# Kernel tuning notes

Measured on AMD Instinct MI355X. Metric: run time of the kernel, lower is better.

Reference implementation:

```python
import jax, jax.numpy as jnp
import numpy as np

INPUT_DIM, HIDDEN_DIM, OUTPUT_DIM = 13, 256, 80


def setup_inputs() -> dict:
    key = jax.random.key(0)
    ks = jax.random.split(key, 5)
    x = jax.random.normal(ks[0], (64, 2048, INPUT_DIM), dtype=jnp.float32)
    # Xavier-uniform init like init_weights(); biases zero.
    def xavier(k, fan_in, fan_out):
        lim = np.sqrt(6.0 / (fan_in + fan_out)).astype(np.float32)
        return jax.random.uniform(k, (fan_in, fan_out), jnp.float32, -lim, lim)
    W1 = xavier(ks[1], INPUT_DIM, HIDDEN_DIM)
    W2 = xavier(ks[2], HIDDEN_DIM, HIDDEN_DIM)
    W3 = xavier(ks[3], HIDDEN_DIM, HIDDEN_DIM)
    W4 = xavier(ks[4], HIDDEN_DIM, OUTPUT_DIM)
    b1 = jnp.zeros((HIDDEN_DIM,), jnp.float32)
    b2 = jnp.zeros((HIDDEN_DIM,), jnp.float32)
    b3 = jnp.zeros((HIDDEN_DIM,), jnp.float32)
    b4 = jnp.zeros((OUTPUT_DIM,), jnp.float32)
    return {"x": x, "W1": W1, "b1": b1, "W2": W2, "b2": b2,
            "W3": W3, "b3": b3, "W4": W4, "b4": b4}


def reference(x, W1, b1, W2, b2, W3, b3, W4, b4):
    # Original loops over timesteps, but each timestep is an identical
    # Linear+ReLU stack -> collapse batch*seq into one batched matmul chain.
    h = jax.nn.relu(jnp.einsum('bsi,ih->bsh', x, W1) + b1)   # encoder L1
    h = jax.nn.relu(jnp.einsum('bsh,hk->bsk', h, W2) + b2)   # encoder L2
    h = jax.nn.relu(jnp.einsum('bsh,hk->bsk', h, W3) + b3)   # decoder L1
    out = jnp.einsum('bsh,ho->bso', h, W4) + b4              # decoder L2 (no ReLU)
    return out
```

## Files before the change

kernel.cpp:

```cpp
#include <hip/hip_runtime.h>


typedef _Float16 half_t;
typedef _Float16 half8 __attribute__((ext_vector_type(8)));
typedef float f32x16 __attribute__((ext_vector_type(16)));
typedef unsigned int uint4v __attribute__((ext_vector_type(4)));
typedef int int2v __attribute__((ext_vector_type(2)));

#define M_TOTAL (64*2048)

__global__ void prep_w(const float* __restrict__ W1, const float* __restrict__ W2,
                       const float* __restrict__ W3, const float* __restrict__ W4,
                       half_t* __restrict__ wp) {
    int tid = blockIdx.x * 256 + threadIdx.x;
    if (tid >= 312 * 512) return;
    int blk = tid >> 9, r = tid & 511;
    int lane = r >> 3, j = r & 7;
    const float* W; int K, N, nt, ks;
    if (blk < 8)        { W = W1; K = 13;  N = 256; nt = blk;              ks = 0; }
    else if (blk < 136) { W = W2; K = 256; N = 256; nt = (blk-8) >> 4;     ks = (blk-8) & 15; }
    else if (blk < 264) { W = W3; K = 256; N = 256; nt = (blk-136) >> 4;   ks = (blk-136) & 15; }
    else                { W = W4; K = 256; N = 80;  nt = (blk-264) >> 4;   ks = (blk-264) & 15; }
    int k = ks * 16 + (lane >> 5) * 8 + j;
    int n = nt * 32 + (lane & 31);
    float v = (k < K && n < N) ? W[k * N + n] : 0.f;
    wp[tid] = (half_t)v;
}


__device__ __forceinline__ unsigned int pkrtz(float a, float b) {
    auto p = __builtin_amdgcn_cvt_pkrtz(a, b);
    return __builtin_bit_cast(unsigned int, p);
}

typedef const __attribute__((address_space(1))) unsigned int guint_t;
typedef __attribute__((address_space(3))) unsigned int luint_t;

__device__ __forceinline__ void stage_strip(const half_t* __restrict__ g,
                                            half_t* l, int bytes, int tid) {
    const char* gc = (const char*)g;
    char* lc = (char*)l;
    const int go = tid * 16;
    const int lo = (tid >> 6) << 10;
#pragma unroll
    for (int r = 0; r < bytes; r += 8192) {
        __builtin_amdgcn_global_load_lds((guint_t*)(gc + r + go),
                                         (luint_t*)(lc + r + lo), 16, 0, 0);
    }
}

__device__ __forceinline__ int strip_off(int s) {
    if (s == 0)  return 0;
    if (s <= 8)  return (8   + (s - 1)  * 16) * 512;
    if (s <= 16) return (136 + (s - 9)  * 16) * 512;
    return (264 + (s - 17) * 16) * 512;
}

#define PIPE_BAR(Nstr) do {                                   \
    asm volatile("s_waitcnt vmcnt(" Nstr ")" ::: "memory");   \
    __builtin_amdgcn_sched_barrier(0);                        \
    __builtin_amdgcn_s_barrier();                             \
    __builtin_amdgcn_sched_barrier(0);                        \
} while (0)

template <int NKS, bool RELU>
__device__ __forceinline__ void dense_tile(const half_t* astrip,
                                           const unsigned int (&Bin)[16][4],
                                           unsigned int (*Bout)[4],
                                           const float* biasnt, int lane, bool hi)
{
    f32x16 acc = {};
    __builtin_amdgcn_s_setprio(1);
#pragma unroll
    for (int ks = 0; ks < NKS; ++ks) {
        half8 a = *(const half8*)(astrip + ((ks * 64 + lane) << 3));
        uint4v bw = { Bin[ks][0], Bin[ks][1], Bin[ks][2], Bin[ks][3] };
        acc = __builtin_amdgcn_mfma_f32_32x32x16_f16(a, __builtin_bit_cast(half8, bw),
                                                     acc, 0, 0, 0);
    }
    __builtin_amdgcn_s_setprio(0);
#pragma unroll
    for (int s = 0; s < 2; ++s) {
        float v[8];
#pragma unroll
        for (int q = 0; q < 8; ++q) {
            int f = (q & 3) + 8 * (q >> 2) + (hi ? 4 : 0);
            float t = acc[8 * s + q] + biasnt[16 * s + f];
            v[q] = RELU ? fmaxf(t, 0.f) : t;
        }
        unsigned int P0 = pkrtz(v[0], v[1]);
        unsigned int P1 = pkrtz(v[2], v[3]);
        unsigned int P2 = pkrtz(v[4], v[5]);
        unsigned int P3 = pkrtz(v[6], v[7]);
        int2v r02 = __builtin_amdgcn_permlane32_swap((int)P0, (int)P2, false, false);
        int2v r13 = __builtin_amdgcn_permlane32_swap((int)P1, (int)P3, false, false);
        Bout[s][0] = (unsigned int)r02.x;
        Bout[s][1] = (unsigned int)r13.x;
        Bout[s][2] = (unsigned int)r02.y;
        Bout[s][3] = (unsigned int)r13.y;
    }
}

__device__ __forceinline__ void out_tile(const half_t* astrip,
                                         const unsigned int (&Bin)[16][4],
                                         const float* biasnt, float* __restrict__ out,
                                         int m0, int nt, int lane, bool hi)
{
    f32x16 acc = {};
    __builtin_amdgcn_s_setprio(1);
#pragma unroll
    for (int ks = 0; ks < 16; ++ks) {
        half8 a = *(const half8*)(astrip + ((ks * 64 + lane) << 3));
        uint4v bw = { Bin[ks][0], Bin[ks][1], Bin[ks][2], Bin[ks][3] };
        acc = __builtin_amdgcn_mfma_f32_32x32x16_f16(a, __builtin_bit_cast(half8, bw),
                                                     acc, 0, 0, 0);
    }
    __builtin_amdgcn_s_setprio(0);
    float* orow = out + (long)(m0 + (lane & 31)) * 80 + nt * 32;
#pragma unroll
    for (int reg = 0; reg < 16; ++reg) {
        if (nt == 2 && (reg >> 2) >= 2) continue;
        int rr = (reg & 3) + 8 * (reg >> 2) + (hi ? 4 : 0);
        orow[rr] = acc[reg] + biasnt[rr];
    }
}

__global__ __launch_bounds__(512, 2) void mlp_mfma(
    const float* __restrict__ x, const half_t* __restrict__ wp,
    const float* __restrict__ b1, const float* __restrict__ b2,
    const float* __restrict__ b3, const float* __restrict__ b4,
    float* __restrict__ out)
{
    __shared__ half_t wbuf[3][8192];
    __shared__ float  bias_lds[864];

    const int tid  = threadIdx.x;
    const int lane = tid & 63;
    const bool hi  = lane >= 32;
    const int m0   = (blockIdx.x * 8 + (tid >> 6)) * 32;

    if (tid < 256) {
        bias_lds[tid] = b1[tid];
        bias_lds[256 + tid] = b2[tid];
        bias_lds[512 + tid] = b3[tid];
    } else if (tid < 352) {
        int t = tid - 256;
        bias_lds[768 + t] = (t < 80) ? b4[t] : 0.f;
    }

    stage_strip(wp + strip_off(0), wbuf[0], 8192, tid);
    stage_strip(wp + strip_off(1), wbuf[1], 16384, tid);

    unsigned int BA[16][4], BB[16][4];

    {
        const float* xp = x + (long)(m0 + (lane & 31)) * 13;
        float xv[8];
        if (!hi) {
#pragma unroll
            for (int j = 0; j < 8; ++j) xv[j] = xp[j];
        } else {
#pragma unroll
            for (int j = 0; j < 5; ++j) xv[j] = xp[8 + j];
            xv[5] = xv[6] = xv[7] = 0.f;
        }
        BA[0][0] = pkrtz(xv[0], xv[1]);
        BA[0][1] = pkrtz(xv[2], xv[3]);
        BA[0][2] = pkrtz(xv[4], xv[5]);
        BA[0][3] = pkrtz(xv[6], xv[7]);
    }

    __syncthreads();

    stage_strip(wp + strip_off(2), wbuf[2], 16384, tid);
#pragma unroll
    for (int nt = 0; nt < 8; ++nt)
        dense_tile<1, true>(&wbuf[0][nt * 512], BA, &BB[2 * nt],
                            bias_lds + nt * 32, lane, hi);

#pragma unroll
    for (int i = 0; i < 8; ++i) {
        const int k = 1 + i;
        PIPE_BAR("2");
        stage_strip(wp + strip_off(k + 2), wbuf[(k + 2) % 3], 16384, tid);
        dense_tile<16, true>(&wbuf[k % 3][0], BB, &BA[2 * i],
                             bias_lds + 256 + i * 32, lane, hi);
    }

#pragma unroll
    for (int i = 0; i < 8; ++i) {
        const int k = 9 + i;
        PIPE_BAR("2");
        stage_strip(wp + strip_off(k + 2), wbuf[(k + 2) % 3], 16384, tid);
        dense_tile<16, true>(&wbuf[k % 3][0], BA, &BB[2 * i],
                             bias_lds + 512 + i * 32, lane, hi);
    }

#pragma unroll
    for (int i = 0; i < 3; ++i) {
        const int k = 17 + i;
        if (i < 2) PIPE_BAR("2");
        else       PIPE_BAR("0");
        if (i == 0) stage_strip(wp + strip_off(19), wbuf[19 % 3], 16384, tid);
        out_tile(&wbuf[k % 3][0], BB, bias_lds + 768 + i * 32, out, m0, i, lane, hi);
    }
}


extern "C" void kernel_launch(void* const* d_in, const int* in_sizes, int n_in,
                              void* d_out, int out_size, void* d_ws, size_t ws_size,
                              hipStream_t stream) {
    const float* x  = (const float*)d_in[0];
    const float* W1 = (const float*)d_in[1];
    const float* b1 = (const float*)d_in[2];
    const float* W2 = (const float*)d_in[3];
    const float* b2 = (const float*)d_in[4];
    const float* W3 = (const float*)d_in[5];
    const float* b3 = (const float*)d_in[6];
    const float* W4 = (const float*)d_in[7];
    const float* b4 = (const float*)d_in[8];
    float* out = (float*)d_out;

    half_t* wp = (half_t*)d_ws;

    hipLaunchKernelGGL(prep_w, dim3(624), dim3(256), 0, stream, W1, W2, W3, W4, wp);
    hipLaunchKernelGGL(mlp_mfma, dim3(M_TOTAL / 256), dim3(512), 0, stream,
                       x, wp, b1, b2, b3, b4, out);
}
```

Measured before the change: 54.21 us.

## Fold biases into MFMA via augmented K, use 1024-thread blocks with half-layer staging

Biases are folded into the weight matrices as an extra K row, paired with a constant-one input column, and applied through an additional MFMA per tile, so the separate bias LDS loads and adds go away. Blocks grow to 1024 threads (16 waves, 512 rows), which halves how many times each block stages the weights. Staging now moves half a layer (4 N-tiles) per step into a 2-buffer, roughly 144 KB LDS, replacing the triple-buffered per-strip pipeline, so there are fewer barriers. In exchange there is less overlap between loads and compute, since every step waits on vmcnt(0), occupancy drops to one block per CU, and each tile does about 6% more MFMA work.

```diff
diff --git a/kernel.cpp b/kernel.cpp
--- a/kernel.cpp
+++ b/kernel.cpp
@@ -8,22 +8,33 @@
 typedef int int2v __attribute__((ext_vector_type(2)));
 
 #define M_TOTAL (64*2048)
-
-__global__ void prep_w(const float* __restrict__ W1, const float* __restrict__ W2,
-                       const float* __restrict__ W3, const float* __restrict__ W4,
+#define NBLK 331
+
+#define L2_OFF (8*512)
+#define L3_OFF (144*512)
+#define L4_OFF (280*512)
+#define HSTRIP (17*4*512)
+
+__global__ void prep_w(const float* __restrict__ W1, const float* __restrict__ b1,
+                       const float* __restrict__ W2, const float* __restrict__ b2,
+                       const float* __restrict__ W3, const float* __restrict__ b3,
+                       const float* __restrict__ W4, const float* __restrict__ b4,
                        half_t* __restrict__ wp) {
     int tid = blockIdx.x * 256 + threadIdx.x;
-    if (tid >= 312 * 512) return;
-    int blk = tid >> 9, r = tid & 511;
-    int lane = r >> 3, j = r & 7;
-    const float* W; int K, N, nt, ks;
-    if (blk < 8)        { W = W1; K = 13;  N = 256; nt = blk;              ks = 0; }
-    else if (blk < 136) { W = W2; K = 256; N = 256; nt = (blk-8) >> 4;     ks = (blk-8) & 15; }
-    else if (blk < 264) { W = W3; K = 256; N = 256; nt = (blk-136) >> 4;   ks = (blk-136) & 15; }
-    else                { W = W4; K = 256; N = 80;  nt = (blk-264) >> 4;   ks = (blk-264) & 15; }
+    if (tid >= NBLK * 512) return;
+    int blk = tid >> 9, r = tid & 511, lane = r >> 3, j = r & 7;
+    const float* W; const float* bias; int K, N, nt, ks;
+    if (blk < 8)        { W = W1; bias = b1; K = 13;  N = 256; nt = blk; ks = 0; }
+    else if (blk < 144) { int b = blk - 8;   W = W2; bias = b2; K = 256; N = 256; nt = b / 17; ks = b % 17; }
+    else if (blk < 280) { int b = blk - 144; W = W3; bias = b3; K = 256; N = 256; nt = b / 17; ks = b % 17; }
+    else                { int b = blk - 280; W = W4; bias = b4; K = 256; N = 80;  nt = b / 17; ks = b % 17; }
     int k = ks * 16 + (lane >> 5) * 8 + j;
     int n = nt * 32 + (lane & 31);
-    float v = (k < K && n < N) ? W[k * N + n] : 0.f;
+    float v = 0.f;
+    if (n < N) {
+        if (k < K)       v = W[k * N + n];
+        else if (k == K) v = bias[n];
+    }
     wp[tid] = (half_t)v;
 }
 
@@ -36,56 +47,47 @@
 typedef const __attribute__((address_space(1))) unsigned int guint_t;
 typedef __attribute__((address_space(3))) unsigned int luint_t;
 
-__device__ __forceinline__ void stage_strip(const half_t* __restrict__ g,
-                                            half_t* l, int bytes, int tid) {
+__device__ __forceinline__ void stage(const half_t* __restrict__ g,
+                                      half_t* l, int bytes, int tid) {
     const char* gc = (const char*)g;
     char* lc = (char*)l;
     const int go = tid * 16;
     const int lo = (tid >> 6) << 10;
-#pragma unroll
-    for (int r = 0; r < bytes; r += 8192) {
+    int r = 0;
+#pragma unroll
+    for (; r + 16384 <= bytes; r += 16384)
         __builtin_amdgcn_global_load_lds((guint_t*)(gc + r + go),
                                          (luint_t*)(lc + r + lo), 16, 0, 0);
-    }
-}
-
-__device__ __forceinline__ int strip_off(int s) {
-    if (s == 0)  return 0;
-    if (s <= 8)  return (8   + (s - 1)  * 16) * 512;
-    if (s <= 16) return (136 + (s - 9)  * 16) * 512;
-    return (264 + (s - 17) * 16) * 512;
-}
-
-#define PIPE_BAR(Nstr) do {                                   \
-    asm volatile("s_waitcnt vmcnt(" Nstr ")" ::: "memory");   \
+    if ((bytes & 16383) && go < (bytes & 16383))
+        __builtin_amdgcn_global_load_lds((guint_t*)(gc + r + go),
+                                         (luint_t*)(lc + r + lo), 16, 0, 0);
+}
+
+#define PIPE_BAR0 do {                                        \
+    asm volatile("s_waitcnt vmcnt(0)" ::: "memory");          \
     __builtin_amdgcn_sched_barrier(0);                        \
     __builtin_amdgcn_s_barrier();                             \
     __builtin_amdgcn_sched_barrier(0);                        \
 } while (0)
 
-template <int NKS, bool RELU>
-__device__ __forceinline__ void dense_tile(const half_t* astrip,
-                                           const unsigned int (&Bin)[16][4],
-                                           unsigned int (*Bout)[4],
-                                           const float* biasnt, int lane, bool hi)
+#define MFMA16(a, b, c) __builtin_amdgcn_mfma_f32_32x32x16_f16((a), (b), (c), 0, 0, 0)
+
+__device__ __forceinline__ half8 bw_cast(const unsigned int* w) {
+    uint4v t = { w[0], w[1], w[2], w[3] };
+    return __builtin_bit_cast(half8, t);
+}
+
+template <bool RELU>
+__device__ __forceinline__ void repack2(const f32x16& acc, bool hi,
+                                        unsigned int* B0, unsigned int* B1)
 {
-    f32x16 acc = {};
-    __builtin_amdgcn_s_setprio(1);
-#pragma unroll
-    for (int ks = 0; ks < NKS; ++ks) {
-        half8 a = *(const half8*)(astrip + ((ks * 64 + lane) << 3));
-        uint4v bw = { Bin[ks][0], Bin[ks][1], Bin[ks][2], Bin[ks][3] };
-        acc = __builtin_amdgcn_mfma_f32_32x32x16_f16(a, __builtin_bit_cast(half8, bw),
-                                                     acc, 0, 0, 0);
-    }
-    __builtin_amdgcn_s_setprio(0);
 #pragma unroll
     for (int s = 0; s < 2; ++s) {
+        unsigned int* Bw = s ? B1 : B0;
         float v[8];
 #pragma unroll
         for (int q = 0; q < 8; ++q) {
-            int f = (q & 3) + 8 * (q >> 2) + (hi ? 4 : 0);
-            float t = acc[8 * s + q] + biasnt[16 * s + f];
+            float t = acc[8 * s + q];
             v[q] = RELU ? fmaxf(t, 0.f) : t;
         }
         unsigned int P0 = pkrtz(v[0], v[1]);
@@ -94,65 +96,57 @@
         unsigned int P3 = pkrtz(v[6], v[7]);
         int2v r02 = __builtin_amdgcn_permlane32_swap((int)P0, (int)P2, false, false);
         int2v r13 = __builtin_amdgcn_permlane32_swap((int)P1, (int)P3, false, false);
-        Bout[s][0] = (unsigned int)r02.x;
-        Bout[s][1] = (unsigned int)r13.x;
-        Bout[s][2] = (unsigned int)r02.y;
-        Bout[s][3] = (unsigned int)r13.y;
-    }
-}
-
-__device__ __forceinline__ void out_tile(const half_t* astrip,
-                                         const unsigned int (&Bin)[16][4],
-                                         const float* biasnt, float* __restrict__ out,
-                                         int m0, int nt, int lane, bool hi)
+        Bw[0] = (unsigned int)r02.x;
+        Bw[1] = (unsigned int)r13.x;
+        Bw[2] = (unsigned int)r02.y;
+        Bw[3] = (unsigned int)r13.y;
+    }
+}
+
+template <bool RELU>
+__device__ __forceinline__ void dense4(const half_t* rg,
+                                       const unsigned int (&Bin)[16][4],
+                                       unsigned int (&Bout)[16][4],
+                                       int ntbase, int lane, bool hi,
+                                       unsigned int cw)
 {
-    f32x16 acc = {};
-    __builtin_amdgcn_s_setprio(1);
-#pragma unroll
-    for (int ks = 0; ks < 16; ++ks) {
-        half8 a = *(const half8*)(astrip + ((ks * 64 + lane) << 3));
-        uint4v bw = { Bin[ks][0], Bin[ks][1], Bin[ks][2], Bin[ks][3] };
-        acc = __builtin_amdgcn_mfma_f32_32x32x16_f16(a, __builtin_bit_cast(half8, bw),
-                                                     acc, 0, 0, 0);
-    }
-    __builtin_amdgcn_s_setprio(0);
-    float* orow = out + (long)(m0 + (lane & 31)) * 80 + nt * 32;
-#pragma unroll
-    for (int reg = 0; reg < 16; ++reg) {
-        if (nt == 2 && (reg >> 2) >= 2) continue;
-        int rr = (reg & 3) + 8 * (reg >> 2) + (hi ? 4 : 0);
-        orow[rr] = acc[reg] + biasnt[rr];
-    }
-}
-
-__global__ __launch_bounds__(512, 2) void mlp_mfma(
+#pragma unroll
+    for (int t = 0; t < 4; ++t) {
+        const half_t* astrip = rg + t * 17 * 512;
+        f32x16 acc = {};
+        __builtin_amdgcn_s_setprio(1);
+#pragma unroll
+        for (int ks = 0; ks < 16; ++ks) {
+            half8 a = *(const half8*)(astrip + ((ks * 64 + lane) << 3));
+            acc = MFMA16(a, bw_cast(Bin[ks]), acc);
+        }
+        {
+            half8 a = *(const half8*)(astrip + ((16 * 64 + lane) << 3));
+            uint4v cb = { cw, 0u, 0u, 0u };
+            acc = MFMA16(a, __builtin_bit_cast(half8, cb), acc);
+        }
+        __builtin_amdgcn_s_setprio(0);
+        repack2<RELU>(acc, hi, Bout[2 * (ntbase + t)], Bout[2 * (ntbase + t) + 1]);
+    }
+}
+
+__global__ __launch_bounds__(1024, 1) void mlp_mfma(
     const float* __restrict__ x, const half_t* __restrict__ wp,
-    const float* __restrict__ b1, const float* __restrict__ b2,
-    const float* __restrict__ b3, const float* __restrict__ b4,
     float* __restrict__ out)
 {
-    __shared__ half_t wbuf[3][8192];
-    __shared__ float  bias_lds[864];
+    __shared__ half_t lds[73728];
 
     const int tid  = threadIdx.x;
     const int lane = tid & 63;
+    const int wave = tid >> 6;
     const bool hi  = lane >= 32;
-    const int m0   = (blockIdx.x * 8 + (tid >> 6)) * 32;
-
-    if (tid < 256) {
-        bias_lds[tid] = b1[tid];
-        bias_lds[256 + tid] = b2[tid];
-        bias_lds[512 + tid] = b3[tid];
-    } else if (tid < 352) {
-        int t = tid - 256;
-        bias_lds[768 + t] = (t < 80) ? b4[t] : 0.f;
-    }
-
-    stage_strip(wp + strip_off(0), wbuf[0], 8192, tid);
-    stage_strip(wp + strip_off(1), wbuf[1], 16384, tid);
-
-    unsigned int BA[16][4], BB[16][4];
-
+    const int m0   = blockIdx.x * 512 + wave * 32;
+    const unsigned int cw = hi ? 0u : 0x3C00u;
+
+    stage(wp,          lds,         8192,  tid);
+    stage(wp + L2_OFF, lds + 4096,  69632, tid);
+
+    unsigned int Bx[4];
     {
         const float* xp = x + (long)(m0 + (lane & 31)) * 13;
         float xv[8];
@@ -162,47 +156,68 @@
         } else {
 #pragma unroll
             for (int j = 0; j < 5; ++j) xv[j] = xp[8 + j];
-            xv[5] = xv[6] = xv[7] = 0.f;
-        }
-        BA[0][0] = pkrtz(xv[0], xv[1]);
-        BA[0][1] = pkrtz(xv[2], xv[3]);
-        BA[0][2] = pkrtz(xv[4], xv[5]);
-        BA[0][3] = pkrtz(xv[6], xv[7]);
-    }
-
-    __syncthreads();
-
-    stage_strip(wp + strip_off(2), wbuf[2], 16384, tid);
-#pragma unroll
-    for (int nt = 0; nt < 8; ++nt)
-        dense_tile<1, true>(&wbuf[0][nt * 512], BA, &BB[2 * nt],
-                            bias_lds + nt * 32, lane, hi);
-
-#pragma unroll
-    for (int i = 0; i < 8; ++i) {
-        const int k = 1 + i;
-        PIPE_BAR("2");
-        stage_strip(wp + strip_off(k + 2), wbuf[(k + 2) % 3], 16384, tid);
-        dense_tile<16, true>(&wbuf[k % 3][0], BB, &BA[2 * i],
-                             bias_lds + 256 + i * 32, lane, hi);
-    }
-
-#pragma unroll
-    for (int i = 0; i < 8; ++i) {
-        const int k = 9 + i;
-        PIPE_BAR("2");
-        stage_strip(wp + strip_off(k + 2), wbuf[(k + 2) % 3], 16384, tid);
-        dense_tile<16, true>(&wbuf[k % 3][0], BA, &BB[2 * i],
-                             bias_lds + 512 + i * 32, lane, hi);
-    }
-
-#pragma unroll
-    for (int i = 0; i < 3; ++i) {
-        const int k = 17 + i;
-        if (i < 2) PIPE_BAR("2");
-        else       PIPE_BAR("0");
-        if (i == 0) stage_strip(wp + strip_off(19), wbuf[19 % 3], 16384, tid);
-        out_tile(&wbuf[k % 3][0], BB, bias_lds + 768 + i * 32, out, m0, i, lane, hi);
+            xv[5] = 1.0f;
+            xv[6] = xv[7] = 0.f;
+        }
+        Bx[0] = pkrtz(xv[0], xv[1]);
+        Bx[1] = pkrtz(xv[2], xv[3]);
+        Bx[2] = pkrtz(xv[4], xv[5]);
+        Bx[3] = pkrtz(xv[6], xv[7]);
+    }
+
+    PIPE_BAR0;
+
+    unsigned int BA[16][4], BB[16][4];
+
+    stage(wp + L2_OFF + HSTRIP, lds + 38912, 69632, tid);
+    {
+        half8 bx = bw_cast(Bx);
+#pragma unroll
+        for (int nt = 0; nt < 8; ++nt) {
+            half8 a = *(const half8*)(lds + nt * 512 + (lane << 3));
+            f32x16 acc = {};
+            acc = MFMA16(a, bx, acc);
+            repack2<true>(acc, hi, BB[2 * nt], BB[2 * nt + 1]);
+        }
+    }
+    dense4<true>(lds + 4096, BB, BA, 0, lane, hi, cw);
+    PIPE_BAR0;
+
+    stage(wp + L3_OFF, lds + 4096, 69632, tid);
+    dense4<true>(lds + 38912, BB, BA, 4, lane, hi, cw);
+    PIPE_BAR0;
+
+    stage(wp + L3_OFF + HSTRIP, lds + 38912, 69632, tid);
+    dense4<true>(lds + 4096, BA, BB, 0, lane, hi, cw);
+    PIPE_BAR0;
+
+    stage(wp + L4_OFF, lds + 4096, 52224, tid);
+    dense4<true>(lds + 38912, BA, BB, 4, lane, hi, cw);
+    PIPE_BAR0;
+
+#pragma unroll
+    for (int t = 0; t < 3; ++t) {
+        const half_t* astrip = lds + 4096 + t * 17 * 512;
+        f32x16 acc = {};
+        __builtin_amdgcn_s_setprio(1);
+#pragma unroll
+        for (int ks = 0; ks < 16; ++ks) {
+            half8 a = *(const half8*)(astrip + ((ks * 64 + lane) << 3));
+            acc = MFMA16(a, bw_cast(BB[ks]), acc);
+        }
+        {
+            half8 a = *(const half8*)(astrip + ((16 * 64 + lane) << 3));
+            uint4v cb = { cw, 0u, 0u, 0u };
+            acc = MFMA16(a, __builtin_bit_cast(half8, cb), acc);
+        }
+        __builtin_amdgcn_s_setprio(0);
+        float* orow = out + (long)(m0 + (lane & 31)) * 80 + t * 32;
+#pragma unroll
+        for (int reg = 0; reg < 16; ++reg) {
+            if (t == 2 && (reg >> 2) >= 2) continue;
+            int rr = (reg & 3) + 8 * (reg >> 2) + (hi ? 4 : 0);
+            orow[rr] = acc[reg];
+        }
     }
 }
 
@@ -223,7 +238,8 @@
 
     half_t* wp = (half_t*)d_ws;
 
-    hipLaunchKernelGGL(prep_w, dim3(624), dim3(256), 0, stream, W1, W2, W3, W4, wp);
-    hipLaunchKernelGGL(mlp_mfma, dim3(M_TOTAL / 256), dim3(512), 0, stream,
-                       x, wp, b1, b2, b3, b4, out);
-}
+    hipLaunchKernelGGL(prep_w, dim3((NBLK * 512 + 255) / 256), dim3(256), 0, stream,
+                       W1, b1, W2, b2, W3, b3, W4, b4, wp);
+    hipLaunchKernelGGL(mlp_mfma, dim3(M_TOTAL / 512), dim3(1024), 0, stream,
+                       x, wp, out);
+}
```

Result: slower. 83.65 us (+54.3%).
